# Kernel optimization log

Hardware: AMD Instinct MI355X
Metric: run time of the kernel (lower is better)

## Reference

```python
import jax, jax.numpy as jnp
import numpy as np

N = 10000      # num nodes
D = 128        # in_channels == out_channels (x is fed back each step)
E1 = 320000    # edges for TAGConv
E2 = 320000    # edges for Transformer_Block
STEPS = 5      # gd_steps


def setup_inputs() -> dict:
    key = jax.random.key(0)
    ks = jax.random.split(key, 8)
    x = jax.random.normal(ks[0], (N, D), dtype=jnp.float32)
    edge_index = jax.random.randint(ks[1], (2, E1), 0, N)
    edge_index_2 = jax.random.randint(ks[2], (2, E2), 0, N)
    s = 0.02  # small init keeps the un-normalized attention unroll numerically sane
    W0 = jax.random.normal(ks[3], (D, D), dtype=jnp.float32) * s  # TAGConv lin for hop-0
    W1 = jax.random.normal(ks[4], (D, D), dtype=jnp.float32) * s  # TAGConv lin for hop-1 (A x)
    Wq = jax.random.normal(ks[5], (D, D), dtype=jnp.float32) * s
    Wk = jax.random.normal(ks[6], (D, D), dtype=jnp.float32) * s
    Wv = jax.random.normal(ks[7], (D, D), dtype=jnp.float32) * s
    return {"x": x, "edge_index": edge_index, "edge_index_2": edge_index_2,
            "W0": W0, "W1": W1, "Wq": Wq, "Wk": Wk, "Wv": Wv}


def reference(x, edge_index, edge_index_2, W0, W1, Wq, Wk, Wv):
    src, dst = edge_index[0], edge_index[1]        # message flows src -> dst
    src2, dst2 = edge_index_2[0], edge_index_2[1]

    def gd_step(h, _):
        # TAGConv(K=1, normalize=False, bias=False): W0 h + W1 (A h)
        agg = jax.ops.segment_sum(h[src], dst, num_segments=N)   # [N, D] sum over in-neighbors
        x1 = h @ W0 + agg @ W1
        # Transformer_Block (graph attention over edge_index_2, use_softmax=False):
        # alpha_ij = <q_i, k_j> on edges, out_i = sum_j alpha_ij * v_j
        Q, K, V = h @ Wq, h @ Wk, h @ Wv
        alpha = jnp.sum(Q[dst2] * K[src2], axis=-1)              # [E2] raw scores, no softmax
        x2 = jax.ops.segment_sum(alpha[:, None] * V[src2], dst2, num_segments=N)
        return x1 - x2, None

    out, _ = jax.lax.scan(gd_step, x, None, length=STEPS)
    return out
```

## Files before the change

### kernel.cpp

```cpp
#include <hip/hip_runtime.h>

#define D 128
#define CAP 96

typedef __attribute__((ext_vector_type(8))) short bf16x8;
typedef __attribute__((ext_vector_type(4))) float f32x4;

__device__ __forceinline__ unsigned short f2bf(float f) {
  union { float f; unsigned int u; } c; c.f = f;
  unsigned int u = c.u;
  unsigned int r = (u + 0x7fffu + ((u >> 16) & 1u)) >> 16;
  return (unsigned short)r;
}
__device__ __forceinline__ float bf2f(unsigned short h) {
  return __uint_as_float(((unsigned int)h) << 16);
}
__device__ __forceinline__ float bf_lo(unsigned int w) {
  return __uint_as_float(w << 16);
}
__device__ __forceinline__ float bf_hi(unsigned int w) {
  return __uint_as_float(w & 0xffff0000u);
}
__device__ __forceinline__ void split2(float a, float b, unsigned int& hi, unsigned int& lo) {
  unsigned short ha = f2bf(a), hb = f2bf(b);
  unsigned short la = f2bf(a - bf2f(ha)), lb = f2bf(b - bf2f(hb));
  hi = (unsigned int)ha | ((unsigned int)hb << 16);
  lo = (unsigned int)la | ((unsigned int)lb << 16);
}

__device__ __forceinline__ void frag_write(unsigned short* __restrict__ Afh,
                                           unsigned short* __restrict__ Afl,
                                           int t, int r, int k, float a, float b) {
  unsigned int hh, hl;
  split2(a, b, hh, hl);
  int s = k >> 5, ksub = (k & 31) >> 3, e = k & 7;
  size_t addr = ((size_t)(t * 12 + s) * 64 + r + 16 * ksub) * 8 + e;
  *(unsigned int*)&Afh[addr] = hh;
  *(unsigned int*)&Afl[addr] = hl;
}

__device__ void gemm_tile(
    const unsigned short* __restrict__ Afh, const unsigned short* __restrict__ Afl,
    int ksteps,
    const unsigned short* __restrict__ Bfh, const unsigned short* __restrict__ Bfl,
    int outcol0, float* __restrict__ C, int ldc,
    unsigned short* __restrict__ Hb, int N, int ntiles, int log2ny, int wgid) {
  const int w = threadIdx.x >> 6, l = threadIdx.x & 63;
  const int wr = w & 1, wc = w >> 1;
  const int rowblk = wgid >> log2ny;
  const int panel = wgid - (rowblk << log2ny);
  const int rowbase = rowblk * 64 + wr * 32;
  const int ntg0 = panel * 4 + wc * 2;

  int t_[2];
#pragma unroll
  for (int tr = 0; tr < 2; ++tr) {
    int t = (rowbase >> 4) + tr;
    t_[tr] = (t < ntiles) ? t : (ntiles - 1);
  }

  const size_t loff = (size_t)l * 8;
  const unsigned short* ah[2];
  const unsigned short* al[2];
#pragma unroll
  for (int tr = 0; tr < 2; ++tr) {
    ah[tr] = Afh + (size_t)t_[tr] * 12 * 512 + loff;
    al[tr] = Afl + (size_t)t_[tr] * 12 * 512 + loff;
  }
  const unsigned short* bh[2];
  const unsigned short* bl[2];
#pragma unroll
  for (int nt = 0; nt < 2; ++nt) {
    bh[nt] = Bfh + (size_t)(ntg0 + nt) * ksteps * 512 + loff;
    bl[nt] = Bfl + (size_t)(ntg0 + nt) * ksteps * 512 + loff;
  }

  f32x4 acc[2][2] = {};
  for (int s = 0; s < ksteps; ++s) {
    bf16x8 Ah[2], Al[2], Bh[2], Bl[2];
#pragma unroll
    for (int tr = 0; tr < 2; ++tr) {
      Ah[tr] = *(const bf16x8*)(ah[tr] + (size_t)s * 512);
      Al[tr] = *(const bf16x8*)(al[tr] + (size_t)s * 512);
    }
#pragma unroll
    for (int nt = 0; nt < 2; ++nt) {
      Bh[nt] = *(const bf16x8*)(bh[nt] + (size_t)s * 512);
      Bl[nt] = *(const bf16x8*)(bl[nt] + (size_t)s * 512);
    }
#pragma unroll
    for (int nt = 0; nt < 2; ++nt) {
#pragma unroll
      for (int tr = 0; tr < 2; ++tr) {
        acc[tr][nt] = __builtin_amdgcn_mfma_f32_16x16x32_bf16(Ah[tr], Bh[nt], acc[tr][nt], 0, 0, 0);
        acc[tr][nt] = __builtin_amdgcn_mfma_f32_16x16x32_bf16(Ah[tr], Bl[nt], acc[tr][nt], 0, 0, 0);
        acc[tr][nt] = __builtin_amdgcn_mfma_f32_16x16x32_bf16(Al[tr], Bh[nt], acc[tr][nt], 0, 0, 0);
      }
    }
  }

  const int r4 = 4 * (l >> 4), cc = (l & 15);
#pragma unroll
  for (int tr = 0; tr < 2; ++tr) {
#pragma unroll
    for (int nt = 0; nt < 2; ++nt) {
      int col = outcol0 + (ntg0 + nt) * 16 + cc;
#pragma unroll
      for (int rr = 0; rr < 4; ++rr) {
        int row = rowbase + tr * 16 + r4 + rr;
        if (row < N) {
          float v = acc[tr][nt][rr];
          C[(size_t)row * ldc + col] = v;
          if (Hb && col < 128) Hb[(size_t)row * D + col] = f2bf(v);
        }
      }
    }
  }
}

__global__ __launch_bounds__(256) void k1_pre1(
    const float* __restrict__ Wq, const float* __restrict__ Wk,
    const float* __restrict__ W0, const float* __restrict__ W1,
    const float* __restrict__ Wv,
    float* __restrict__ M, float* __restrict__ Wc,
    int* __restrict__ cnt, int twoN) {
  int gid = blockIdx.x * 256 + threadIdx.x;
  if (gid < twoN) cnt[gid] = 0;
  int bx = blockIdx.x;
  if (bx < 64) {
    int r = bx * 2 + (threadIdx.x >> 7);
    int c = threadIdx.x & 127;
    float acc = 0.f;
    for (int d = 0; d < D; ++d) acc += Wq[r * D + d] * Wk[c * D + d];
    M[r * D + c] = acc;
  } else {
    int idx = (bx - 64) * 256 + threadIdx.x;
    int r = idx >> 7, c = idx & 127;
    float v;
    if (r < 128) v = W0[r * D + c];
    else if (r < 256) v = W1[(r - 128) * D + c];
    else v = -Wv[(r - 256) * D + c];
    Wc[idx] = v;
  }
}

__global__ __launch_bounds__(256) void k2_fill_pre2(
    const int* __restrict__ src1, const int* __restrict__ dst1,
    int* __restrict__ cnt1, int* __restrict__ slot1, int E1,
    const int* __restrict__ src2, const int* __restrict__ dst2,
    int* __restrict__ cnt2, int* __restrict__ slot2, int E2, int ebt,
    const float* __restrict__ Wc, const float* __restrict__ M,
    float* __restrict__ WM) {
  if (blockIdx.x < (unsigned)ebt) {
    int e = blockIdx.x * 256 + threadIdx.x;
    if (e < E1) {
      int d = dst1[e];
      int pos = atomicAdd(&cnt1[d], 1);
      if (pos < CAP) slot1[d * CAP + pos] = src1[e];
    }
    int e2 = e - E1;
    if (e2 >= 0 && e2 < E2) {
      int d = dst2[e2];
      int pos = atomicAdd(&cnt2[d], 1);
      if (pos < CAP) slot2[d * CAP + pos] = src2[e2];
    }
  } else {
    int idx = (blockIdx.x - ebt) * 256 + threadIdx.x;
    if (idx >= 384 * D) return;
    int r = idx >> 7, c = idx & 127;
    float acc = 0.f;
    for (int k = 0; k < D; ++k) acc += Wc[r * D + k] * M[k * D + c];
    WM[idx] = acc;
  }
}

__global__ __launch_bounds__(256) void k3_pre3cvt(
    const float* __restrict__ x,
    unsigned short* __restrict__ Afh, unsigned short* __restrict__ Afl,
    unsigned short* __restrict__ Hb, int ncvt,
    const float* __restrict__ Wc, const float* __restrict__ WM,
    const float* __restrict__ M,
    unsigned short* __restrict__ Bfh, unsigned short* __restrict__ Bfl,
    unsigned short* __restrict__ Mfh, unsigned short* __restrict__ Mfl) {
  int gid = blockIdx.x * 256 + threadIdx.x;
  if (gid < ncvt) {
    int row = gid >> 6, f = (gid & 63) * 2;
    float2 v = *(const float2*)&x[row * D + f];
    frag_write(Afh, Afl, row >> 4, row & 15, f, v.x, v.y);
    unsigned int p = (unsigned int)f2bf(v.x) | ((unsigned int)f2bf(v.y) << 16);
    *(unsigned int*)&Hb[(size_t)row * D + f] = p;
    return;
  }
  int idx = gid - ncvt;
  if (idx < 16 * 12 * 512) {
    int e = idx & 7, l = (idx >> 3) & 63;
    int s = (idx >> 9) % 12, ntg = idx / (12 * 512);
    int n2 = ntg * 16 + (l & 15);
    int k = s * 32 + (l >> 4) * 8 + e;
    float v = (n2 < 128) ? Wc[k * D + n2] : WM[k * D + (n2 - 128)];
    unsigned short h = f2bf(v);
    Bfh[idx] = h;
    Bfl[idx] = f2bf(v - bf2f(h));
  } else {
    int i2 = idx - 16 * 12 * 512;
    if (i2 >= 8 * 4 * 512) return;
    int e = i2 & 7, l = (i2 >> 3) & 63;
    int s = (i2 >> 9) & 3, ntg = i2 / (4 * 512);
    int n2 = ntg * 16 + (l & 15);
    int k = s * 32 + (l >> 4) * 8 + e;
    float v = M[k * D + n2];
    unsigned short h = f2bf(v);
    Mfh[i2] = h;
    Mfl[i2] = f2bf(v - bf2f(h));
  }
}

__global__ __launch_bounds__(256) void agg_k(
    const float* __restrict__ h, int ldh,
    const float* __restrict__ qt,
    const unsigned short* __restrict__ Hb,
    const int* __restrict__ cnt1, const int* __restrict__ slot1,
    const int* __restrict__ cnt2, const int* __restrict__ slot2,
    unsigned short* __restrict__ Afh, unsigned short* __restrict__ Afl, int N) {
  int gw = (int)((blockIdx.x * blockDim.x + threadIdx.x) >> 6);
  if (gw >= N) return;
  const int i = __builtin_amdgcn_readfirstlane(gw);
  const int l = threadIdx.x & 63;
  const int m = l & 15, g = l >> 4;
  const int c0 = m * 8;

  float q[8];
  *(float4*)&q[0] = *(const float4*)&qt[(size_t)i * 256 + c0];
  *(float4*)&q[4] = *(const float4*)&qt[(size_t)i * 256 + c0 + 4];

  float a1[8] = {0.f, 0.f, 0.f, 0.f, 0.f, 0.f, 0.f, 0.f};
  float a2[8] = {0.f, 0.f, 0.f, 0.f, 0.f, 0.f, 0.f, 0.f};

  {
    const int* sp = slot1 + (size_t)i * CAP;
    int end = cnt1[i]; if (end > CAP) end = CAP;
    int nj[4]; bool nv[4];
#pragma unroll
    for (int u = 0; u < 4; ++u) {
      int ee = 4 * u + g;
      nv[u] = ee < end; nj[u] = nv[u] ? sp[ee] : 0;
    }
    for (int e = 0; e < end; e += 16) {
      int j[4]; bool v[4];
#pragma unroll
      for (int u = 0; u < 4; ++u) { j[u] = nj[u]; v[u] = nv[u]; }
      int en = e + 16;
      if (en < end) {
#pragma unroll
        for (int u = 0; u < 4; ++u) {
          int ee = en + 4 * u + g;
          nv[u] = ee < end; nj[u] = nv[u] ? sp[ee] : 0;
        }
      }
      uint4 w[4];
#pragma unroll
      for (int u = 0; u < 4; ++u)
        w[u] = *(const uint4*)&Hb[(size_t)j[u] * D + c0];
#pragma unroll
      for (int u = 0; u < 4; ++u) {
        if (!v[u]) w[u] = make_uint4(0u, 0u, 0u, 0u);
        a1[0] += bf_lo(w[u].x); a1[1] += bf_hi(w[u].x);
        a1[2] += bf_lo(w[u].y); a1[3] += bf_hi(w[u].y);
        a1[4] += bf_lo(w[u].z); a1[5] += bf_hi(w[u].z);
        a1[6] += bf_lo(w[u].w); a1[7] += bf_hi(w[u].w);
      }
    }
  }

  {
    const int* sp = slot2 + (size_t)i * CAP;
    int end = cnt2[i]; if (end > CAP) end = CAP;
    int nj[4]; bool nv[4];
#pragma unroll
    for (int u = 0; u < 4; ++u) {
      int ee = 4 * u + g;
      nv[u] = ee < end; nj[u] = nv[u] ? sp[ee] : 0;
    }
    for (int e = 0; e < end; e += 16) {
      int j[4]; bool v[4];
#pragma unroll
      for (int u = 0; u < 4; ++u) { j[u] = nj[u]; v[u] = nv[u]; }
      int en = e + 16;
      if (en < end) {
#pragma unroll
        for (int u = 0; u < 4; ++u) {
          int ee = en + 4 * u + g;
          nv[u] = ee < end; nj[u] = nv[u] ? sp[ee] : 0;
        }
      }
      uint4 w[4];
#pragma unroll
      for (int u = 0; u < 4; ++u)
        w[u] = *(const uint4*)&Hb[(size_t)j[u] * D + c0];
      float fv[4][8]; float p[4];
#pragma unroll
      for (int u = 0; u < 4; ++u) {
        if (!v[u]) w[u] = make_uint4(0u, 0u, 0u, 0u);
        fv[u][0] = bf_lo(w[u].x); fv[u][1] = bf_hi(w[u].x);
        fv[u][2] = bf_lo(w[u].y); fv[u][3] = bf_hi(w[u].y);
        fv[u][4] = bf_lo(w[u].z); fv[u][5] = bf_hi(w[u].z);
        fv[u][6] = bf_lo(w[u].w); fv[u][7] = bf_hi(w[u].w);
        p[u] = q[0] * fv[u][0] + q[1] * fv[u][1] + q[2] * fv[u][2] + q[3] * fv[u][3] +
               q[4] * fv[u][4] + q[5] * fv[u][5] + q[6] * fv[u][6] + q[7] * fv[u][7];
      }
#pragma unroll
      for (int ofs = 1; ofs < 16; ofs <<= 1) {
#pragma unroll
        for (int u = 0; u < 4; ++u) p[u] += __shfl_xor(p[u], ofs);
      }
#pragma unroll
      for (int u = 0; u < 4; ++u)
#pragma unroll
        for (int t = 0; t < 8; ++t) a2[t] += p[u] * fv[u][t];
    }
  }

#pragma unroll
  for (int t = 0; t < 8; ++t) {
    a1[t] += __shfl_xor(a1[t], 16); a1[t] += __shfl_xor(a1[t], 32);
    a2[t] += __shfl_xor(a2[t], 16); a2[t] += __shfl_xor(a2[t], 32);
  }

  if (g < 3) {
    float vals[8];
    if (g == 0) {
      *(float4*)&vals[0] = *(const float4*)&h[(size_t)i * ldh + c0];
      *(float4*)&vals[4] = *(const float4*)&h[(size_t)i * ldh + c0 + 4];
    } else if (g == 1) {
#pragma unroll
      for (int t = 0; t < 8; ++t) vals[t] = a1[t];
    } else {
#pragma unroll
      for (int t = 0; t < 8; ++t) vals[t] = a2[t];
    }
    uint4 hiw, low;
    split2(vals[0], vals[1], hiw.x, low.x);
    split2(vals[2], vals[3], hiw.y, low.y);
    split2(vals[4], vals[5], hiw.z, low.z);
    split2(vals[6], vals[7], hiw.w, low.w);
    size_t base = (((size_t)(i >> 4) * 12 + g * 4 + (m >> 2)) * 64 +
                   (i & 15) + 16 * (m & 3)) * 8;
    *(uint4*)&Afh[base] = hiw;
    *(uint4*)&Afl[base] = low;
  }
}

__global__ __launch_bounds__(256) void gemm_mfma(
    const unsigned short* __restrict__ Afh, const unsigned short* __restrict__ Afl,
    int ksteps,
    const unsigned short* __restrict__ Bfh, const unsigned short* __restrict__ Bfl,
    int outcol0, float* __restrict__ C, int ldc,
    unsigned short* __restrict__ Hb, int N, int ntiles, int log2ny) {
  const int nwg = gridDim.x;
  const int flat = blockIdx.x;
  const int xcd = flat & 7;
  const int qq = nwg >> 3, rr8 = nwg & 7;
  const int wgid = (xcd < rr8 ? xcd * (qq + 1) : rr8 * (qq + 1) + (xcd - rr8) * qq) + (flat >> 3);
  gemm_tile(Afh, Afl, ksteps, Bfh, Bfl, outcol0, C, ldc, Hb, N, ntiles, log2ny, wgid);
}


extern "C" void kernel_launch(void* const* d_in, const int* in_sizes, int n_in,
                              void* d_out, int out_size, void* d_ws, size_t ws_size,
                              hipStream_t stream) {
  const float* x  = (const float*)d_in[0];
  const int* ei1  = (const int*)d_in[1];
  const int* ei2  = (const int*)d_in[2];
  const float* W0 = (const float*)d_in[3];
  const float* W1 = (const float*)d_in[4];
  const float* Wq = (const float*)d_in[5];
  const float* Wk = (const float*)d_in[6];
  const float* Wv = (const float*)d_in[7];

  const int N  = in_sizes[0] / D;
  const int E1 = in_sizes[1] / 2;
  const int E2 = in_sizes[2] / 2;
  const int* src1 = ei1;
  const int* dst1 = ei1 + E1;
  const int* src2 = ei2;
  const int* dst2 = ei2 + E2;
  const int TILES = (N + 15) / 16;

  float* Cbuf = (float*)d_ws;
  float* M    = Cbuf + (size_t)N * 256;
  float* Wc   = M + 16384;
  float* WM   = Wc + 49152;
  unsigned short* Afh = (unsigned short*)(WM + 49152);
  unsigned short* Afl = Afh + (size_t)TILES * 6144;
  unsigned short* Bfh = Afl + (size_t)TILES * 6144;
  unsigned short* Bfl = Bfh + 98304;
  unsigned short* Mfh = Bfl + 98304;
  unsigned short* Mfl = Mfh + 16384;
  unsigned short* Hb  = Mfl + 16384;
  int* cnt1  = (int*)(Hb + (size_t)N * D);
  int* cnt2  = cnt1 + N;
  int* slot1 = cnt2 + N;
  int* slot2 = slot1 + (size_t)N * CAP;

  size_t needed = ((size_t)N * 256 + 16384 + 2 * 49152) * 4ull +
                  ((size_t)2 * TILES * 6144 + 2 * 98304 + 2 * 16384 + (size_t)N * D) * 2ull +
                  ((size_t)2 * N + 2ull * N * CAP) * 4ull;
  if (ws_size < needed) return;

  float* out = (float*)d_out;

  const int ebt = (E1 + E2 + 255) / 256;
  const int gx = (N + 63) / 64;
  const int ablocks = (N * 64 + 255) / 256;
  const int ncvt = N * 64;
  const int tot3 = ncvt + 16 * 12 * 512 + 8 * 4 * 512;

  k1_pre1<<<256, 256, 0, stream>>>(Wq, Wk, W0, W1, Wv, M, Wc, cnt1, 2 * N);
  k2_fill_pre2<<<ebt + 192, 256, 0, stream>>>(src1, dst1, cnt1, slot1, E1,
                                              src2, dst2, cnt2, slot2, E2, ebt,
                                              Wc, M, WM);
  k3_pre3cvt<<<(tot3 + 255) / 256, 256, 0, stream>>>(x, Afh, Afl, Hb, ncvt,
                                                     Wc, WM, M, Bfh, Bfl, Mfh, Mfl);
  gemm_mfma<<<gx * 2, 256, 0, stream>>>(Afh, Afl, 4, Mfh, Mfl,
                                        128, Cbuf, 256, nullptr, N, TILES, 1);

  for (int s = 0; s < 5; ++s) {
    const float* hsrc = (s == 0) ? x : Cbuf;
    const int ldh = (s == 0) ? D : 256;

    agg_k<<<ablocks, 256, 0, stream>>>(hsrc, ldh, Cbuf + 128, Hb,
                                       cnt1, slot1, cnt2, slot2, Afh, Afl, N);

    if (s == 4) {
      gemm_mfma<<<gx * 2, 256, 0, stream>>>(Afh, Afl, 12, Bfh, Bfl,
                                            0, out, D, nullptr, N, TILES, 1);
    } else {
      gemm_mfma<<<gx * 4, 256, 0, stream>>>(Afh, Afl, 12, Bfh, Bfl,
                                            0, Cbuf, 256, Hb, N, TILES, 2);
    }
  }
}
```

Baseline: 259.4 us.

## Partition slot fill by destination range and interleave both edge-list gathers

The edge bucketing kernel now uses 1024 blocks in 8 groups. Each group scans all edges with a grid stride and only inserts edges whose destination falls in its eighth of the node range. The aim is to localise atomics and slot writes, possibly to the same XCD or cache region, at the cost of each edge being read eight times. The aggregation kernel now walks both neighbour lists in a single fused loop, issuing both sets of gathers together to raise memory-level parallelism, with wasted iterations when the two degrees differ.

```diff
diff --git a/kernel.cpp b/kernel.cpp
--- a/kernel.cpp
+++ b/kernel.cpp
@@ -148,24 +148,34 @@
     const int* __restrict__ src1, const int* __restrict__ dst1,
     int* __restrict__ cnt1, int* __restrict__ slot1, int E1,
     const int* __restrict__ src2, const int* __restrict__ dst2,
-    int* __restrict__ cnt2, int* __restrict__ slot2, int E2, int ebt,
+    int* __restrict__ cnt2, int* __restrict__ slot2, int E2, int nfb,
     const float* __restrict__ Wc, const float* __restrict__ M,
-    float* __restrict__ WM) {
-  if (blockIdx.x < (unsigned)ebt) {
-    int e = blockIdx.x * 256 + threadIdx.x;
-    if (e < E1) {
+    float* __restrict__ WM, int N) {
+  if (blockIdx.x < (unsigned)nfb) {
+    const int grp = blockIdx.x & 7;
+    const int bid = blockIdx.x >> 3;
+    const int nbg = nfb >> 3;
+    const int rng = (N + 7) >> 3;
+    const int rlo = grp * rng;
+    const int rhi = (rlo + rng < N) ? rlo + rng : N;
+    const int tid = bid * 256 + threadIdx.x;
+    const int stride = nbg * 256;
+    for (int e = tid; e < E1; e += stride) {
       int d = dst1[e];
-      int pos = atomicAdd(&cnt1[d], 1);
-      if (pos < CAP) slot1[d * CAP + pos] = src1[e];
-    }
-    int e2 = e - E1;
-    if (e2 >= 0 && e2 < E2) {
-      int d = dst2[e2];
-      int pos = atomicAdd(&cnt2[d], 1);
-      if (pos < CAP) slot2[d * CAP + pos] = src2[e2];
+      if (d >= rlo && d < rhi) {
+        int pos = atomicAdd(&cnt1[d], 1);
+        if (pos < CAP) slot1[d * CAP + pos] = src1[e];
+      }
+    }
+    for (int e = tid; e < E2; e += stride) {
+      int d = dst2[e];
+      if (d >= rlo && d < rhi) {
+        int pos = atomicAdd(&cnt2[d], 1);
+        if (pos < CAP) slot2[d * CAP + pos] = src2[e];
+      }
     }
   } else {
-    int idx = (blockIdx.x - ebt) * 256 + threadIdx.x;
+    int idx = (blockIdx.x - nfb) * 256 + threadIdx.x;
     if (idx >= 384 * D) return;
     int r = idx >> 7, c = idx & 127;
     float acc = 0.f;
@@ -236,88 +246,69 @@
   float a1[8] = {0.f, 0.f, 0.f, 0.f, 0.f, 0.f, 0.f, 0.f};
   float a2[8] = {0.f, 0.f, 0.f, 0.f, 0.f, 0.f, 0.f, 0.f};
 
-  {
-    const int* sp = slot1 + (size_t)i * CAP;
-    int end = cnt1[i]; if (end > CAP) end = CAP;
-    int nj[4]; bool nv[4];
+  const int* sp1 = slot1 + (size_t)i * CAP;
+  const int* sp2 = slot2 + (size_t)i * CAP;
+  int end1 = cnt1[i]; if (end1 > CAP) end1 = CAP;
+  int end2 = cnt2[i]; if (end2 > CAP) end2 = CAP;
+  const int maxe = (end1 > end2) ? end1 : end2;
+
+  int nj1[4], nj2[4]; bool nv1[4], nv2[4];
+#pragma unroll
+  for (int u = 0; u < 4; ++u) {
+    int ee = 4 * u + g;
+    nv1[u] = ee < end1; nj1[u] = nv1[u] ? sp1[ee] : 0;
+    nv2[u] = ee < end2; nj2[u] = nv2[u] ? sp2[ee] : 0;
+  }
+
+  for (int e = 0; e < maxe; e += 16) {
+    int j1[4], j2[4]; bool v1[4], v2[4];
 #pragma unroll
     for (int u = 0; u < 4; ++u) {
-      int ee = 4 * u + g;
-      nv[u] = ee < end; nj[u] = nv[u] ? sp[ee] : 0;
-    }
-    for (int e = 0; e < end; e += 16) {
-      int j[4]; bool v[4];
-#pragma unroll
-      for (int u = 0; u < 4; ++u) { j[u] = nj[u]; v[u] = nv[u]; }
-      int en = e + 16;
-      if (en < end) {
-#pragma unroll
-        for (int u = 0; u < 4; ++u) {
-          int ee = en + 4 * u + g;
-          nv[u] = ee < end; nj[u] = nv[u] ? sp[ee] : 0;
-        }
+      j1[u] = nj1[u]; v1[u] = nv1[u];
+      j2[u] = nj2[u]; v2[u] = nv2[u];
+    }
+    uint4 w1[4], w2[4];
+#pragma unroll
+    for (int u = 0; u < 4; ++u) w1[u] = *(const uint4*)&Hb[(size_t)j1[u] * D + c0];
+#pragma unroll
+    for (int u = 0; u < 4; ++u) w2[u] = *(const uint4*)&Hb[(size_t)j2[u] * D + c0];
+    int en = e + 16;
+    if (en < maxe) {
+#pragma unroll
+      for (int u = 0; u < 4; ++u) {
+        int ee = en + 4 * u + g;
+        nv1[u] = ee < end1; nj1[u] = nv1[u] ? sp1[ee] : 0;
+        nv2[u] = ee < end2; nj2[u] = nv2[u] ? sp2[ee] : 0;
       }
-      uint4 w[4];
-#pragma unroll
-      for (int u = 0; u < 4; ++u)
-        w[u] = *(const uint4*)&Hb[(size_t)j[u] * D + c0];
-#pragma unroll
-      for (int u = 0; u < 4; ++u) {
-        if (!v[u]) w[u] = make_uint4(0u, 0u, 0u, 0u);
-        a1[0] += bf_lo(w[u].x); a1[1] += bf_hi(w[u].x);
-        a1[2] += bf_lo(w[u].y); a1[3] += bf_hi(w[u].y);
-        a1[4] += bf_lo(w[u].z); a1[5] += bf_hi(w[u].z);
-        a1[6] += bf_lo(w[u].w); a1[7] += bf_hi(w[u].w);
-      }
-    }
-  }
-
-  {
-    const int* sp = slot2 + (size_t)i * CAP;
-    int end = cnt2[i]; if (end > CAP) end = CAP;
-    int nj[4]; bool nv[4];
+    }
 #pragma unroll
     for (int u = 0; u < 4; ++u) {
-      int ee = 4 * u + g;
-      nv[u] = ee < end; nj[u] = nv[u] ? sp[ee] : 0;
-    }
-    for (int e = 0; e < end; e += 16) {
-      int j[4]; bool v[4];
-#pragma unroll
-      for (int u = 0; u < 4; ++u) { j[u] = nj[u]; v[u] = nv[u]; }
-      int en = e + 16;
-      if (en < end) {
-#pragma unroll
-        for (int u = 0; u < 4; ++u) {
-          int ee = en + 4 * u + g;
-          nv[u] = ee < end; nj[u] = nv[u] ? sp[ee] : 0;
-        }
-      }
-      uint4 w[4];
-#pragma unroll
-      for (int u = 0; u < 4; ++u)
-        w[u] = *(const uint4*)&Hb[(size_t)j[u] * D + c0];
-      float fv[4][8]; float p[4];
-#pragma unroll
-      for (int u = 0; u < 4; ++u) {
-        if (!v[u]) w[u] = make_uint4(0u, 0u, 0u, 0u);
-        fv[u][0] = bf_lo(w[u].x); fv[u][1] = bf_hi(w[u].x);
-        fv[u][2] = bf_lo(w[u].y); fv[u][3] = bf_hi(w[u].y);
-        fv[u][4] = bf_lo(w[u].z); fv[u][5] = bf_hi(w[u].z);
-        fv[u][6] = bf_lo(w[u].w); fv[u][7] = bf_hi(w[u].w);
-        p[u] = q[0] * fv[u][0] + q[1] * fv[u][1] + q[2] * fv[u][2] + q[3] * fv[u][3] +
-               q[4] * fv[u][4] + q[5] * fv[u][5] + q[6] * fv[u][6] + q[7] * fv[u][7];
-      }
-#pragma unroll
-      for (int ofs = 1; ofs < 16; ofs <<= 1) {
-#pragma unroll
-        for (int u = 0; u < 4; ++u) p[u] += __shfl_xor(p[u], ofs);
-      }
-#pragma unroll
-      for (int u = 0; u < 4; ++u)
-#pragma unroll
-        for (int t = 0; t < 8; ++t) a2[t] += p[u] * fv[u][t];
-    }
+      if (!v1[u]) w1[u] = make_uint4(0u, 0u, 0u, 0u);
+      a1[0] += bf_lo(w1[u].x); a1[1] += bf_hi(w1[u].x);
+      a1[2] += bf_lo(w1[u].y); a1[3] += bf_hi(w1[u].y);
+      a1[4] += bf_lo(w1[u].z); a1[5] += bf_hi(w1[u].z);
+      a1[6] += bf_lo(w1[u].w); a1[7] += bf_hi(w1[u].w);
+    }
+    float fv[4][8]; float p[4];
+#pragma unroll
+    for (int u = 0; u < 4; ++u) {
+      if (!v2[u]) w2[u] = make_uint4(0u, 0u, 0u, 0u);
+      fv[u][0] = bf_lo(w2[u].x); fv[u][1] = bf_hi(w2[u].x);
+      fv[u][2] = bf_lo(w2[u].y); fv[u][3] = bf_hi(w2[u].y);
+      fv[u][4] = bf_lo(w2[u].z); fv[u][5] = bf_hi(w2[u].z);
+      fv[u][6] = bf_lo(w2[u].w); fv[u][7] = bf_hi(w2[u].w);
+      p[u] = q[0] * fv[u][0] + q[1] * fv[u][1] + q[2] * fv[u][2] + q[3] * fv[u][3] +
+             q[4] * fv[u][4] + q[5] * fv[u][5] + q[6] * fv[u][6] + q[7] * fv[u][7];
+    }
+#pragma unroll
+    for (int ofs = 1; ofs < 16; ofs <<= 1) {
+#pragma unroll
+      for (int u = 0; u < 4; ++u) p[u] += __shfl_xor(p[u], ofs);
+    }
+#pragma unroll
+    for (int u = 0; u < 4; ++u)
+#pragma unroll
+      for (int t = 0; t < 8; ++t) a2[t] += p[u] * fv[u][t];
   }
 
 #pragma unroll
@@ -409,16 +400,16 @@
 
   float* out = (float*)d_out;
 
-  const int ebt = (E1 + E2 + 255) / 256;
   const int gx = (N + 63) / 64;
   const int ablocks = (N * 64 + 255) / 256;
   const int ncvt = N * 64;
   const int tot3 = ncvt + 16 * 12 * 512 + 8 * 4 * 512;
+  const int nfb = 1024;
 
   k1_pre1<<<256, 256, 0, stream>>>(Wq, Wk, W0, W1, Wv, M, Wc, cnt1, 2 * N);
-  k2_fill_pre2<<<ebt + 192, 256, 0, stream>>>(src1, dst1, cnt1, slot1, E1,
-                                              src2, dst2, cnt2, slot2, E2, ebt,
-                                              Wc, M, WM);
+  k2_fill_pre2<<<nfb + 192, 256, 0, stream>>>(src1, dst1, cnt1, slot1, E1,
+                                              src2, dst2, cnt2, slot2, E2, nfb,
+                                              Wc, M, WM, N);
   k3_pre3cvt<<<(tot3 + 255) / 256, 256, 0, stream>>>(x, Afh, Afl, Hb, ncvt,
                                                      Wc, WM, M, Bfh, Bfl, Mfh, Mfl);
   gemm_mfma<<<gx * 2, 256, 0, stream>>>(Afh, Afl, 4, Mfh, Mfl,
```

After: 269.6 us. +3.9%, slower.

## Spread edge-bucket fill across three preprocessing kernels to overlap with setup work

Applied to the files above, without the earlier changes.

The atomic edge-to-slot bucketing, which previously ran entirely inside the second preprocessing kernel, is split into three chunks (45/35/20 of the edge blocks). The chunks run as extra blocks in k2, in the conversion kernel k3, and in a new kernel that fuses the remaining fill with the initial Q-projection GEMM. The aim is to hide the latency-bound atomic scatter behind independent dense setup work and to remove one launch. Correctness depends on the fill finishing before agg_k, which stream ordering guarantees. The split ratios are fixed heuristics.

```diff
diff --git a/kernel.cpp b/kernel.cpp
--- a/kernel.cpp
+++ b/kernel.cpp
@@ -37,6 +37,25 @@
   size_t addr = ((size_t)(t * 12 + s) * 64 + r + 16 * ksub) * 8 + e;
   *(unsigned int*)&Afh[addr] = hh;
   *(unsigned int*)&Afl[addr] = hl;
+}
+
+__device__ void fill_chunk(int gfb,
+                           const int* __restrict__ src1, const int* __restrict__ dst1,
+                           int* __restrict__ cnt1, int* __restrict__ slot1, int E1,
+                           const int* __restrict__ src2, const int* __restrict__ dst2,
+                           int* __restrict__ cnt2, int* __restrict__ slot2, int E2) {
+  int e = gfb * 256 + threadIdx.x;
+  if (e < E1) {
+    int d = dst1[e];
+    int pos = atomicAdd(&cnt1[d], 1);
+    if (pos < CAP) slot1[d * CAP + pos] = src1[e];
+  }
+  int e2 = e - E1;
+  if (e2 >= 0 && e2 < E2) {
+    int d = dst2[e2];
+    int pos = atomicAdd(&cnt2[d], 1);
+    if (pos < CAP) slot2[d * CAP + pos] = src2[e2];
+  }
 }
 
 __device__ void gemm_tile(
@@ -148,24 +167,14 @@
     const int* __restrict__ src1, const int* __restrict__ dst1,
     int* __restrict__ cnt1, int* __restrict__ slot1, int E1,
     const int* __restrict__ src2, const int* __restrict__ dst2,
-    int* __restrict__ cnt2, int* __restrict__ slot2, int E2, int ebt,
+    int* __restrict__ cnt2, int* __restrict__ slot2, int E2, int fb2,
     const float* __restrict__ Wc, const float* __restrict__ M,
     float* __restrict__ WM) {
-  if (blockIdx.x < (unsigned)ebt) {
-    int e = blockIdx.x * 256 + threadIdx.x;
-    if (e < E1) {
-      int d = dst1[e];
-      int pos = atomicAdd(&cnt1[d], 1);
-      if (pos < CAP) slot1[d * CAP + pos] = src1[e];
-    }
-    int e2 = e - E1;
-    if (e2 >= 0 && e2 < E2) {
-      int d = dst2[e2];
-      int pos = atomicAdd(&cnt2[d], 1);
-      if (pos < CAP) slot2[d * CAP + pos] = src2[e2];
-    }
+  if (blockIdx.x < (unsigned)fb2) {
+    fill_chunk(blockIdx.x, src1, dst1, cnt1, slot1, E1,
+               src2, dst2, cnt2, slot2, E2);
   } else {
-    int idx = (blockIdx.x - ebt) * 256 + threadIdx.x;
+    int idx = (blockIdx.x - fb2) * 256 + threadIdx.x;
     if (idx >= 384 * D) return;
     int r = idx >> 7, c = idx & 127;
     float acc = 0.f;
@@ -174,7 +183,12 @@
   }
 }
 
-__global__ __launch_bounds__(256) void k3_pre3cvt(
+__global__ __launch_bounds__(256) void k3_fill_pre3cvt(
+    const int* __restrict__ src1, const int* __restrict__ dst1,
+    int* __restrict__ cnt1, int* __restrict__ slot1, int E1,
+    const int* __restrict__ src2, const int* __restrict__ dst2,
+    int* __restrict__ cnt2, int* __restrict__ slot2, int E2,
+    int fb3, int gfb0,
     const float* __restrict__ x,
     unsigned short* __restrict__ Afh, unsigned short* __restrict__ Afl,
     unsigned short* __restrict__ Hb, int ncvt,
@@ -182,7 +196,12 @@
     const float* __restrict__ M,
     unsigned short* __restrict__ Bfh, unsigned short* __restrict__ Bfl,
     unsigned short* __restrict__ Mfh, unsigned short* __restrict__ Mfl) {
-  int gid = blockIdx.x * 256 + threadIdx.x;
+  if (blockIdx.x < (unsigned)fb3) {
+    fill_chunk(gfb0 + blockIdx.x, src1, dst1, cnt1, slot1, E1,
+               src2, dst2, cnt2, slot2, E2);
+    return;
+  }
+  int gid = (blockIdx.x - fb3) * 256 + threadIdx.x;
   if (gid < ncvt) {
     int row = gid >> 6, f = (gid & 63) * 2;
     float2 v = *(const float2*)&x[row * D + f];
@@ -215,6 +234,24 @@
   }
 }
 
+__global__ __launch_bounds__(256) void k4_fill_qtgemm(
+    const int* __restrict__ src1, const int* __restrict__ dst1,
+    int* __restrict__ cnt1, int* __restrict__ slot1, int E1,
+    const int* __restrict__ src2, const int* __restrict__ dst2,
+    int* __restrict__ cnt2, int* __restrict__ slot2, int E2,
+    int fb4, int gfb0,
+    const unsigned short* __restrict__ Afh, const unsigned short* __restrict__ Afl,
+    const unsigned short* __restrict__ Mfh, const unsigned short* __restrict__ Mfl,
+    float* __restrict__ Cbuf, int N, int ntiles) {
+  if (blockIdx.x < (unsigned)fb4) {
+    fill_chunk(gfb0 + blockIdx.x, src1, dst1, cnt1, slot1, E1,
+               src2, dst2, cnt2, slot2, E2);
+  } else {
+    gemm_tile(Afh, Afl, 4, Mfh, Mfl, 128, Cbuf, 256, nullptr, N, ntiles, 1,
+              blockIdx.x - fb4);
+  }
+}
+
 __global__ __launch_bounds__(256) void agg_k(
     const float* __restrict__ h, int ldh,
     const float* __restrict__ qt,
@@ -409,20 +446,27 @@
 
   float* out = (float*)d_out;
 
-  const int ebt = (E1 + E2 + 255) / 256;
   const int gx = (N + 63) / 64;
   const int ablocks = (N * 64 + 255) / 256;
   const int ncvt = N * 64;
   const int tot3 = ncvt + 16 * 12 * 512 + 8 * 4 * 512;
+  const int k3b = (tot3 + 255) / 256;
+
+  const int ebt = (E1 + E2 + 255) / 256;
+  const int fb2 = (ebt * 45) / 100;
+  const int fb3 = (ebt * 35) / 100;
+  const int fb4 = ebt - fb2 - fb3;
 
   k1_pre1<<<256, 256, 0, stream>>>(Wq, Wk, W0, W1, Wv, M, Wc, cnt1, 2 * N);
-  k2_fill_pre2<<<ebt + 192, 256, 0, stream>>>(src1, dst1, cnt1, slot1, E1,
-                                              src2, dst2, cnt2, slot2, E2, ebt,
+  k2_fill_pre2<<<fb2 + 192, 256, 0, stream>>>(src1, dst1, cnt1, slot1, E1,
+                                              src2, dst2, cnt2, slot2, E2, fb2,
                                               Wc, M, WM);
-  k3_pre3cvt<<<(tot3 + 255) / 256, 256, 0, stream>>>(x, Afh, Afl, Hb, ncvt,
-                                                     Wc, WM, M, Bfh, Bfl, Mfh, Mfl);
-  gemm_mfma<<<gx * 2, 256, 0, stream>>>(Afh, Afl, 4, Mfh, Mfl,
-                                        128, Cbuf, 256, nullptr, N, TILES, 1);
+  k3_fill_pre3cvt<<<fb3 + k3b, 256, 0, stream>>>(
+      src1, dst1, cnt1, slot1, E1, src2, dst2, cnt2, slot2, E2, fb3, fb2,
+      x, Afh, Afl, Hb, ncvt, Wc, WM, M, Bfh, Bfl, Mfh, Mfl);
+  k4_fill_qtgemm<<<fb4 + gx * 2, 256, 0, stream>>>(
+      src1, dst1, cnt1, slot1, E1, src2, dst2, cnt2, slot2, E2, fb4, fb2 + fb3,
+      Afh, Afl, Mfh, Mfl, Cbuf, N, TILES);
 
   for (int s = 0; s < 5; ++s) {
     const float* hsrc = (s == 0) ? x : Cbuf;
```

After: 259.2 us. About the same (-0.1%).
